# Kernel tuning notes

Hardware: AMD Instinct MI355X
Metric: run time of the kernel (lower is better)

Reference implementation:

```python
import jax, jax.numpy as jnp
import numpy as np

B, C, H, W = 4, 512, 64, 208
HID = 512          # params.text_hidden_dim; must equal C for view(1,C,H,-1)
DS = 16            # 1/scale_factor for nearest downsample of the mask
N_REG = 4          # four region-indexed attention modules


def setup_inputs() -> dict:
    key = jax.random.key(0)
    ks = jax.random.split(key, 7)
    image_feature = jax.random.normal(ks[0], (B, C, H, W), dtype=jnp.float32)
    text_feat = jax.random.normal(ks[1], (N_REG, B, HID), dtype=jnp.float32)
    # Mask is constant per (full-res) column so that each region's pixel count
    # is divisible by H, as the original view(1, C, H, -1) requires.
    col_labels = jax.random.randint(ks[2], (B, W * DS), 1, N_REG + 1)
    text_mask = jnp.broadcast_to(
        col_labels[:, None, None, :], (B, 1, H * DS, W * DS)
    ).astype(jnp.int32)
    # Per-region MHA params (nn.Linear weights, no bias assumed).
    Wq = jax.random.normal(ks[3], (N_REG, C, HID), dtype=jnp.float32) * (C ** -0.5)
    Wk = jax.random.normal(ks[4], (N_REG, HID, HID), dtype=jnp.float32) * (HID ** -0.5)
    Wv = jax.random.normal(ks[5], (N_REG, HID, HID), dtype=jnp.float32) * (HID ** -0.5)
    Wo = jax.random.normal(ks[6], (N_REG, HID, C), dtype=jnp.float32) * (HID ** -0.5)
    return {
        "image_feature": image_feature,
        "text_feat": text_feat,
        "text_mask": text_mask,
        "Wq": Wq,
        "Wk": Wk,
        "Wv": Wv,
        "Wo": Wo,
    }


def reference(image_feature, text_feat, text_mask, Wq, Wk, Wv, Wo):
    # F.interpolate(scale=1/16, mode='nearest') == strided slicing for integer stride.
    mask_ds = text_mask[:, 0, ::DS, ::DS]          # [B, H, W]
    col_labels = mask_ds[:, 0, :]                  # [B, W] (mask is column-constant)
    # Cross-attention of every region pixel (query) against ONE text token z
    # (single key/value): softmax over a length-1 axis is identically 1, so
    # attn_out = Wo @ (Wv @ z) for every pixel, and Wq/Wk receive zero gradient.
    # With the residual connection: out_pixel = x_pixel + (z Wv) Wo per region.
    delta = jnp.einsum('rbh,rhd,rdc->brc', text_feat, Wv, Wo)          # [B, R, C]
    d_col = jnp.take_along_axis(delta, (col_labels - 1)[:, :, None], axis=1)  # [B, W, C]
    out = image_feature + d_col.transpose(0, 2, 1)[:, :, None, :]      # [B, C, H, W]
    # The torch code concatenates regions along width in sorted-unique label
    # order, i.e. columns are permuted by (label, original column) -- a stable
    # argsort of the column labels.
    order = jnp.argsort(col_labels, axis=1, stable=True)               # [B, W]
    return jnp.take_along_axis(out, order[:, None, None, :], axis=3)
```

## Files before the change

kernel.cpp:

```cpp
#include <hip/hip_runtime.h>

#define B_ 4
#define C_ 512
#define H_ 64
#define W_ 208
#define HID_ 512
#define NREG_ 4
#define DS_ 16


__global__ __launch_bounds__(256) void prep1_kernel(
    const float* __restrict__ tf, const float* __restrict__ Wv,
    const int* __restrict__ mask, float* __restrict__ tmp, int* __restrict__ swl) {
  int blk = blockIdx.x, tid = threadIdx.x;
  if (blk < 64) {
    int r = blk >> 4;
    int d0 = (blk & 15) * 32;
    __shared__ float tf_s[B_ * HID_];
    __shared__ float red[8][B_][32];
#pragma unroll
    for (int k = 0; k < 8; ++k) {
      int idx = k * 256 + tid;
      tf_s[idx] = tf[r * (B_ * HID_) + idx];
    }
    __syncthreads();
    int hg = tid >> 5, dd = tid & 31;
    float acc[B_] = {};
#pragma unroll 4
    for (int q = 0; q < 64; ++q) {
      int hh = hg * 64 + q;
      float w = Wv[(size_t)(r * HID_ + hh) * HID_ + d0 + dd];
#pragma unroll
      for (int b = 0; b < B_; ++b) acc[b] += tf_s[b * HID_ + hh] * w;
    }
#pragma unroll
    for (int b = 0; b < B_; ++b) red[hg][b][dd] = acc[b];
    __syncthreads();
    if (tid < 128) {
      int b2 = tid >> 5, d2 = tid & 31;
      float s = 0.f;
#pragma unroll
      for (int q = 0; q < 8; ++q) s += red[q][b2][d2];
      tmp[(b2 * NREG_ + r) * HID_ + d0 + d2] = s;
    }
  } else {
    int b = blk - 64;
    const size_t mb = (size_t)b * (H_ * DS_) * (W_ * DS_);
    int w = tid;
    int l = (w < W_) ? (mask[mb + (size_t)w * DS_] - 1) : -1;
    int wave = tid >> 6, lane = tid & 63;
    unsigned long long bal[NREG_];
    __shared__ int wcnt[4][NREG_];
#pragma unroll
    for (int r = 0; r < NREG_; ++r) bal[r] = __ballot(l == r);
    if (lane < NREG_) wcnt[wave][lane] = __popcll(bal[lane]);
    __syncthreads();
    if (w < W_) {
      int pos = 0;
#pragma unroll
      for (int q = 0; q < NREG_; ++q) {
        int tot = wcnt[0][q] + wcnt[1][q] + wcnt[2][q] + wcnt[3][q];
        if (q < l) pos += tot;
      }
#pragma unroll
      for (int v = 0; v < 4; ++v)
        if (v < wave) pos += wcnt[v][l];
      pos += __popcll(bal[l] & ((1ull << lane) - 1ull));
      swl[b * W_ + pos] = w | (l << 16);
    }
  }
}

__global__ __launch_bounds__(256) void prep2_kernel(
    const float* __restrict__ tmp, const float* __restrict__ Wo,
    float* __restrict__ delta) {
  int blk = blockIdx.x, tid = threadIdx.x;
  int r = blk >> 3;
  int c0 = (blk & 7) * 64;
  __shared__ float tmp_s[B_ * HID_];
  __shared__ float red[4][B_][64];
#pragma unroll
  for (int k = 0; k < 8; ++k) {
    int idx = k * 256 + tid;
    int b = idx >> 9, d = idx & 511;
    tmp_s[idx] = tmp[(b * NREG_ + r) * HID_ + d];
  }
  __syncthreads();
  int dg = tid >> 6, cc = tid & 63;
  float acc[B_] = {};
#pragma unroll 4
  for (int q = 0; q < 128; ++q) {
    int d = dg * 128 + q;
    float w = Wo[(size_t)(r * HID_ + d) * C_ + c0 + cc];
#pragma unroll
    for (int b = 0; b < B_; ++b) acc[b] += tmp_s[b * HID_ + d] * w;
  }
#pragma unroll
  for (int b = 0; b < B_; ++b) red[dg][b][cc] = acc[b];
  __syncthreads();
  {
    float s = red[0][dg][cc] + red[1][dg][cc] + red[2][dg][cc] + red[3][dg][cc];
    delta[(dg * NREG_ + r) * C_ + c0 + cc] = s;
  }
}

#define RCH_ (W_ / 4)
__global__ __launch_bounds__(256) void apply_kernel(
    const float* __restrict__ img, const float* __restrict__ delta,
    const int* __restrict__ swl, float* __restrict__ out) {
  int blk = blockIdx.x;
  int b = blk >> 9;
  int c = blk & (C_ - 1);
  int tid = threadIdx.x;
  int wave = tid >> 6, lane = tid & 63;
  __shared__ int swl_s[W_];
  __shared__ float dquad[W_];
  __shared__ float dsel_s[NREG_];
  __shared__ float tile[4][16 * W_];

  const float4* srcv = (const float4*)(img + (size_t)blk * (H_ * W_));
  float4* dstv = (float4*)(out + (size_t)blk * (H_ * W_));
  int off = wave * (16 * RCH_);

  float4 pre[13];
#pragma unroll
  for (int k = 0; k < 13; ++k) pre[k] = srcv[off + k * 64 + lane];

  if (tid < W_) swl_s[tid] = swl[b * W_ + tid];
  if (tid < NREG_) dsel_s[tid] = delta[(b * NREG_ + tid) * C_ + c];
  __syncthreads();
  if (tid < W_) dquad[tid] = dsel_s[swl_s[tid] >> 16];
  __syncthreads();

  float* mytile = &tile[wave][0];
#pragma unroll
  for (int k = 0; k < 13; ++k) {
    ((float4*)mytile)[k * 64 + lane] = pre[k];
  }
  const int4* swl4 = (const int4*)swl_s;
  const float4* dq4 = (const float4*)dquad;
#pragma unroll
  for (int k = 0; k < 13; ++k) {
    int i = k * 64 + lane;
    int hl = i / RCH_;
    int jo = i - hl * RCH_;
    int4 sw = swl4[jo];
    float4 dq = dq4[jo];
    const float* rowp = mytile + hl * W_;
    float4 o;
    o.x = rowp[sw.x & 0xFFFF] + dq.x;
    o.y = rowp[sw.y & 0xFFFF] + dq.y;
    o.z = rowp[sw.z & 0xFFFF] + dq.z;
    o.w = rowp[sw.w & 0xFFFF] + dq.w;
    dstv[off + i] = o;
  }
}

extern "C" void kernel_launch(void* const* d_in, const int* in_sizes, int n_in,
                              void* d_out, int out_size, void* d_ws, size_t ws_size,
                              hipStream_t stream) {
  const float* img  = (const float*)d_in[0];
  const float* tf   = (const float*)d_in[1];
  const int*   mask = (const int*)d_in[2];
  const float* Wv   = (const float*)d_in[5];
  const float* Wo   = (const float*)d_in[6];
  float* tmp   = (float*)d_ws;
  float* delta = (float*)((char*)d_ws + 32768);
  int*   swl   = (int*)((char*)d_ws + 65536);
  float* out   = (float*)d_out;

  prep1_kernel<<<68, 256, 0, stream>>>(tf, Wv, mask, tmp, swl);
  prep2_kernel<<<32, 256, 0, stream>>>(tmp, Wo, delta);
  apply_kernel<<<B_ * C_, 256, 0, stream>>>(img, delta, swl, out);
}
```

Baseline: 277.2 us.

## Load image rows directly into LDS and gather in two waitcnt stages

The apply kernel now copies each wave's image rows straight into shared memory with global_load_lds, so the data no longer passes through registers. The gather phase is split around partial vmcnt waits to overlap the copy with the start of processing. Output stores become nontemporal, and the swl load is vectorised. The main risk is the vmcnt(6) wait: it assumes loads complete in order and that each wave's gather only reads rows already landed, which is fragile given the lane-to-row mapping and the wave-wide LDS write layout.

After: 261.0 us. -5.8%, faster.

```diff
diff --git a/kernel.cpp b/kernel.cpp
--- a/kernel.cpp
+++ b/kernel.cpp
@@ -7,6 +7,9 @@
 #define HID_ 512
 #define NREG_ 4
 #define DS_ 16
+
+typedef float f32x4 __attribute__((ext_vector_type(4)));
+typedef int i32x4 __attribute__((ext_vector_type(4)));
 
 
 __global__ __launch_bounds__(256) void prep1_kernel(
@@ -105,6 +108,11 @@
 }
 
 #define RCH_ (W_ / 4)
+__device__ __forceinline__ void gload_lds16(const float* g, float* l) {
+  __builtin_amdgcn_global_load_lds(
+      (const __attribute__((address_space(1))) void*)g,
+      (__attribute__((address_space(3))) void*)l, 16, 0, 0);
+}
 __global__ __launch_bounds__(256) void apply_kernel(
     const float* __restrict__ img, const float* __restrict__ delta,
     const int* __restrict__ swl, float* __restrict__ out) {
@@ -118,42 +126,44 @@
   __shared__ float dsel_s[NREG_];
   __shared__ float tile[4][16 * W_];
 
-  const float4* srcv = (const float4*)(img + (size_t)blk * (H_ * W_));
-  float4* dstv = (float4*)(out + (size_t)blk * (H_ * W_));
+  const float* srcf = img + (size_t)blk * (H_ * W_);
+  f32x4* dstv = (f32x4*)(out + (size_t)blk * (H_ * W_));
   int off = wave * (16 * RCH_);
+  float* mytile = &tile[wave][0];
 
-  float4 pre[13];
-#pragma unroll
-  for (int k = 0; k < 13; ++k) pre[k] = srcv[off + k * 64 + lane];
-
-  if (tid < W_) swl_s[tid] = swl[b * W_ + tid];
+  if (tid < 52) ((i32x4*)swl_s)[tid] = ((const i32x4*)(swl + b * W_))[tid];
   if (tid < NREG_) dsel_s[tid] = delta[(b * NREG_ + tid) * C_ + c];
   __syncthreads();
   if (tid < W_) dquad[tid] = dsel_s[swl_s[tid] >> 16];
   __syncthreads();
 
-  float* mytile = &tile[wave][0];
 #pragma unroll
-  for (int k = 0; k < 13; ++k) {
-    ((float4*)mytile)[k * 64 + lane] = pre[k];
+  for (int k = 0; k < 13; ++k)
+    gload_lds16(srcf + (size_t)(off + k * 64 + lane) * 4, mytile + k * 256);
+
+  const i32x4* swl4 = (const i32x4*)swl_s;
+  const f32x4* dq4 = (const f32x4*)dquad;
+#define GATHER_CHUNK(k) {                               \
+    int i = (k) * 64 + lane;                            \
+    int hl = i / RCH_;                                  \
+    int jo = i - hl * RCH_;                             \
+    i32x4 sw = swl4[jo];                                \
+    f32x4 dq = dq4[jo];                                 \
+    const float* rowp = mytile + hl * W_;               \
+    f32x4 o;                                            \
+    o.x = rowp[sw.x & 0xFFFF] + dq.x;                   \
+    o.y = rowp[sw.y & 0xFFFF] + dq.y;                   \
+    o.z = rowp[sw.z & 0xFFFF] + dq.z;                   \
+    o.w = rowp[sw.w & 0xFFFF] + dq.w;                   \
+    __builtin_nontemporal_store(o, &dstv[off + i]);     \
   }
-  const int4* swl4 = (const int4*)swl_s;
-  const float4* dq4 = (const float4*)dquad;
+  asm volatile("s_waitcnt vmcnt(6)" ::: "memory");
 #pragma unroll
-  for (int k = 0; k < 13; ++k) {
-    int i = k * 64 + lane;
-    int hl = i / RCH_;
-    int jo = i - hl * RCH_;
-    int4 sw = swl4[jo];
-    float4 dq = dq4[jo];
-    const float* rowp = mytile + hl * W_;
-    float4 o;
-    o.x = rowp[sw.x & 0xFFFF] + dq.x;
-    o.y = rowp[sw.y & 0xFFFF] + dq.y;
-    o.z = rowp[sw.z & 0xFFFF] + dq.z;
-    o.w = rowp[sw.w & 0xFFFF] + dq.w;
-    dstv[off + i] = o;
-  }
+  for (int k = 0; k < 6; ++k) GATHER_CHUNK(k);
+  asm volatile("s_waitcnt vmcnt(0)" ::: "memory");
+#pragma unroll
+  for (int k = 6; k < 13; ++k) GATHER_CHUNK(k);
+#undef GATHER_CHUNK
 }
 
 extern "C" void kernel_launch(void* const* d_in, const int* in_sizes, int n_in,
```

## Rewrite apply kernel as single-wave double-buffered LDS-direct load pipeline

Applied to the files above, without the earlier changes.

The apply kernel now runs one 64-thread wave per block, each handling two (b,c) planes in eight 16-row chunks. Chunks are loaded straight into LDS with global_load_lds and double-buffered, so the next chunk streams in while the current one is permuted and written out. Stores are nontemporal and the per-column deltas come from shuffles instead of an extra sync stage. The price is fewer threads per block, a full vmcnt(0) wait every chunk, and no __syncthreads between LDS writes and reads, which depends on single-wave ordering.

Result: faster. 267.3 us (-3.6%).

```diff
diff --git a/kernel.cpp b/kernel.cpp
--- a/kernel.cpp
+++ b/kernel.cpp
@@ -7,6 +7,9 @@
 #define HID_ 512
 #define NREG_ 4
 #define DS_ 16
+
+typedef float f32x4 __attribute__((ext_vector_type(4)));
+typedef int i32x4 __attribute__((ext_vector_type(4)));
 
 
 __global__ __launch_bounds__(256) void prep1_kernel(
@@ -105,54 +108,90 @@
 }
 
 #define RCH_ (W_ / 4)
-__global__ __launch_bounds__(256) void apply_kernel(
+__device__ __forceinline__ void gload_lds16(const float* g, float* l) {
+  __builtin_amdgcn_global_load_lds(
+      (const __attribute__((address_space(1))) void*)g,
+      (__attribute__((address_space(3))) void*)l, 16, 0, 0);
+}
+__global__ __launch_bounds__(64) void apply_kernel(
     const float* __restrict__ img, const float* __restrict__ delta,
     const int* __restrict__ swl, float* __restrict__ out) {
-  int blk = blockIdx.x;
-  int b = blk >> 9;
-  int c = blk & (C_ - 1);
-  int tid = threadIdx.x;
-  int wave = tid >> 6, lane = tid & 63;
+  int lane = threadIdx.x;
+  int gw = blockIdx.x;
+  int p0 = gw * 2;
+  int b = p0 >> 9;
+  int c0 = p0 & (C_ - 1);
+  __shared__ float tile[2][16 * W_];
   __shared__ int swl_s[W_];
-  __shared__ float dquad[W_];
-  __shared__ float dsel_s[NREG_];
-  __shared__ float tile[4][16 * W_];
-
-  const float4* srcv = (const float4*)(img + (size_t)blk * (H_ * W_));
-  float4* dstv = (float4*)(out + (size_t)blk * (H_ * W_));
-  int off = wave * (16 * RCH_);
-
-  float4 pre[13];
-#pragma unroll
-  for (int k = 0; k < 13; ++k) pre[k] = srcv[off + k * 64 + lane];
-
-  if (tid < W_) swl_s[tid] = swl[b * W_ + tid];
-  if (tid < NREG_) dsel_s[tid] = delta[(b * NREG_ + tid) * C_ + c];
-  __syncthreads();
-  if (tid < W_) dquad[tid] = dsel_s[swl_s[tid] >> 16];
-  __syncthreads();
-
-  float* mytile = &tile[wave][0];
-#pragma unroll
-  for (int k = 0; k < 13; ++k) {
-    ((float4*)mytile)[k * 64 + lane] = pre[k];
-  }
-  const int4* swl4 = (const int4*)swl_s;
-  const float4* dq4 = (const float4*)dquad;
-#pragma unroll
-  for (int k = 0; k < 13; ++k) {
-    int i = k * 64 + lane;
-    int hl = i / RCH_;
-    int jo = i - hl * RCH_;
-    int4 sw = swl4[jo];
-    float4 dq = dq4[jo];
-    const float* rowp = mytile + hl * W_;
-    float4 o;
-    o.x = rowp[sw.x & 0xFFFF] + dq.x;
-    o.y = rowp[sw.y & 0xFFFF] + dq.y;
-    o.z = rowp[sw.z & 0xFFFF] + dq.z;
-    o.w = rowp[sw.w & 0xFFFF] + dq.w;
-    dstv[off + i] = o;
+  __shared__ float dq_s[W_];
+
+  if (lane < 52) ((i32x4*)swl_s)[lane] = ((const i32x4*)(swl + b * W_))[lane];
+
+  float v0 = 0.f, v1 = 0.f;
+  if (lane < NREG_) {
+    v0 = delta[(b * NREG_ + lane) * C_ + c0];
+    v1 = delta[(b * NREG_ + lane) * C_ + c0 + 1];
+  }
+  float e0 = __shfl(v0, 0), e1 = __shfl(v0, 1), e2 = __shfl(v0, 2), e3 = __shfl(v0, 3);
+  float f0 = __shfl(v1, 0), f1 = __shfl(v1, 1), f2 = __shfl(v1, 2), f3 = __shfl(v1, 3);
+#pragma unroll
+  for (int q = 0; q < 4; ++q) {
+    int pos = q * 64 + lane;
+    if (pos < W_) {
+      int lab = swl_s[pos] >> 16;
+      dq_s[pos] = lab == 0 ? e0 : lab == 1 ? e1 : lab == 2 ? e2 : e3;
+    }
+  }
+
+  {
+    const float* src = img + (size_t)p0 * (H_ * W_);
+#pragma unroll
+    for (int k = 0; k < 13; ++k)
+      gload_lds16(src + (k * 64 + lane) * 4, &tile[0][k * 256]);
+  }
+  int cur = 0;
+  const i32x4* swl4 = (const i32x4*)swl_s;
+  const f32x4* dq4 = (const f32x4*)dq_s;
+  for (int u = 0; u < 8; ++u) {
+    asm volatile("s_waitcnt vmcnt(0)" ::: "memory");
+    if (u < 7) {
+      int un = u + 1;
+      const float* srcn =
+          img + ((size_t)(p0 + (un >> 2)) * H_ + (un & 3) * 16) * W_;
+      float* nb = tile[cur ^ 1];
+#pragma unroll
+      for (int k = 0; k < 13; ++k)
+        gload_lds16(srcn + (k * 64 + lane) * 4, &nb[k * 256]);
+    }
+    int p = p0 + (u >> 2), qr = u & 3;
+    f32x4* dstv = (f32x4*)out + ((size_t)p * (H_ * RCH_) + qr * (16 * RCH_));
+    const float* mytile = tile[cur];
+#pragma unroll
+    for (int k = 0; k < 13; ++k) {
+      int i = k * 64 + lane;
+      int hl = i / RCH_;
+      int jo = i - hl * RCH_;
+      i32x4 sw = swl4[jo];
+      f32x4 dq = dq4[jo];
+      const float* rowp = mytile + hl * W_;
+      f32x4 o;
+      o.x = rowp[sw.x & 0xFFFF] + dq.x;
+      o.y = rowp[sw.y & 0xFFFF] + dq.y;
+      o.z = rowp[sw.z & 0xFFFF] + dq.z;
+      o.w = rowp[sw.w & 0xFFFF] + dq.w;
+      __builtin_nontemporal_store(o, &dstv[i]);
+    }
+    if (u == 3) {
+#pragma unroll
+      for (int q = 0; q < 4; ++q) {
+        int pos = q * 64 + lane;
+        if (pos < W_) {
+          int lab = swl_s[pos] >> 16;
+          dq_s[pos] = lab == 0 ? f0 : lab == 1 ? f1 : lab == 2 ? f2 : f3;
+        }
+      }
+    }
+    cur ^= 1;
   }
 }
 
@@ -171,5 +210,5 @@
 
   prep1_kernel<<<68, 256, 0, stream>>>(tf, Wv, mask, tmp, swl);
   prep2_kernel<<<32, 256, 0, stream>>>(tmp, Wo, delta);
-  apply_kernel<<<B_ * C_, 256, 0, stream>>>(img, delta, swl, out);
-}
+  apply_kernel<<<1024, 64, 0, stream>>>(img, delta, swl, out);
+}
```
